# Kernel optimization log

Hardware: AMD Instinct MI355X
Metric: run time of the kernel (lower is better)

## Reference

```python
import jax, jax.numpy as jnp
import numpy as np

B, S, D, DH = 2, 2048, 1024, 64
H = D // DH
EPS = 1e-6

def rms_norm(x):
    # flax RMSNorm, use_scale=False: x / sqrt(mean(x^2) + eps)
    return x * jax.lax.rsqrt(jnp.mean(jnp.square(x), axis=-1, keepdims=True) + EPS)

def setup_inputs() -> dict:
    key = jax.random.key(0)
    ks = jax.random.split(key, 6)
    std = (1.0 / D) ** 0.5
    x = jax.random.normal(ks[0], (B, S, D), dtype=jnp.float32)
    Wq = jax.random.normal(ks[1], (D, D), dtype=jnp.float32) * std
    Wk = jax.random.normal(ks[2], (D, D), dtype=jnp.float32) * std
    Wv = jax.random.normal(ks[3], (D, D), dtype=jnp.float32) * std
    # output_proj is zero-initialized in the original; use small random so
    # backward through it is non-trivial for kernel correctness testing.
    Wo = jax.random.normal(ks[4], (D, D), dtype=jnp.float32) * std
    mask = jnp.tril(jnp.ones((S, S), dtype=bool))[None, None]  # causal [1,1,S,S]
    return {"x": x, "Wq": Wq, "Wk": Wk, "Wv": Wv, "Wo": Wo, "mask": mask}

def reference(x, Wq, Wk, Wv, Wo, mask):
    scale = (1.0 / DH) ** 0.5
    q = (x @ Wq).reshape(B, S, H, DH).transpose(0, 2, 1, 3)  # [B,H,S,DH]
    k = (x @ Wk).reshape(B, S, H, DH).transpose(0, 2, 1, 3)
    v = (x @ Wv).reshape(B, S, H, DH).transpose(0, 2, 1, 3)
    q = rms_norm(q)
    k = rms_norm(k)
    scores = jnp.einsum('bhsd,bhtd->bhst', q, k) * scale
    scores = jnp.where(mask, scores, jnp.finfo(scores.dtype).min)
    probs = jax.nn.softmax(scores, axis=-1)
    out = jnp.einsum('bhst,bhtd->bhsd', probs, v)
    out = out.transpose(0, 2, 1, 3).reshape(B, S, D)
    return out @ Wo
```

## Files before the change

kernel.cpp:

```cpp
#include <hip/hip_runtime.h>
#include <stdint.h>


typedef __attribute__((ext_vector_type(8))) short s16x8;
typedef __attribute__((ext_vector_type(4))) float fx4;
typedef __attribute__((ext_vector_type(4))) unsigned int ux4;
typedef __attribute__((ext_vector_type(2))) unsigned int ux2;

__device__ __forceinline__ unsigned short f2bf(float x) {
  unsigned u = __builtin_bit_cast(unsigned, x);
  u += 0x7fffu + ((u >> 16) & 1u);
  return (unsigned short)(u >> 16);
}
__device__ __forceinline__ float bf2f(unsigned short h) {
  return __builtin_bit_cast(float, (unsigned)h << 16);
}

__device__ __forceinline__ void gload_lds16(const void* g, void* l) {
  __builtin_amdgcn_global_load_lds(
      (const __attribute__((address_space(1))) unsigned int*)g,
      (__attribute__((address_space(3))) unsigned int*)l, 16, 0, 0);
}

__global__ void k_conv_bf16(const float* __restrict__ X,
                            unsigned short* __restrict__ Y, int n4) {
  int stride = gridDim.x * blockDim.x;
  for (int i = blockIdx.x * blockDim.x + threadIdx.x; i < n4; i += stride) {
    fx4 v = *(const fx4*)(X + (size_t)i * 4);
    ux2 o;
    o[0] = (unsigned)f2bf(v[0]) | ((unsigned)f2bf(v[1]) << 16);
    o[1] = (unsigned)f2bf(v[2]) | ((unsigned)f2bf(v[3]) << 16);
    *(ux2*)(Y + (size_t)i * 4) = o;
  }
}

__global__ void k_transpose_w(const float* __restrict__ W0, const float* __restrict__ W1,
                              const float* __restrict__ W2, const float* __restrict__ W3,
                              unsigned short* __restrict__ T0, unsigned short* __restrict__ T1,
                              unsigned short* __restrict__ T2, unsigned short* __restrict__ T3) {
  const float* W = blockIdx.z == 0 ? W0 : blockIdx.z == 1 ? W1 : blockIdx.z == 2 ? W2 : W3;
  unsigned short* T = blockIdx.z == 0 ? T0 : blockIdx.z == 1 ? T1 : blockIdx.z == 2 ? T2 : T3;
  __shared__ float t[32][33];
  int bx = blockIdx.x * 32, by = blockIdx.y * 32;
  int tx = threadIdx.x, ty = threadIdx.y;
#pragma unroll
  for (int i = 0; i < 32; i += 8)
    t[ty + i][tx] = W[(size_t)(by + ty + i) * 1024 + bx + tx];
  __syncthreads();
#pragma unroll
  for (int i = 0; i < 32; i += 8)
    T[(size_t)(bx + ty + i) * 1024 + by + tx] = f2bf(t[tx][ty + i]);
}

template <int OUTF32>
__global__ __launch_bounds__(256, 2)
void k_gemm_bt(const unsigned short* __restrict__ A,
               const unsigned short* __restrict__ W0,
               const unsigned short* __restrict__ W1,
               const unsigned short* __restrict__ W2,
               void* __restrict__ Cptr, int ldc) {
  __shared__ unsigned short As[128 * 64];
  __shared__ unsigned short Bs[128 * 64];
  const int tid = threadIdx.x;
  const int w = tid >> 6, l = tid & 63;
  const int lr = l & 15, lg = l >> 4;
  const int wm = w >> 1, wn = w & 1;
  const int m0 = blockIdx.x * 128;
  const int nt = blockIdx.y;
  const unsigned short* Bt = (nt < 8) ? W0 : (nt < 16) ? W1 : W2;
  const int n0 = (nt & 7) * 128;

  fx4 acc[4][4] = {};

  const int srow = w * 8 + (l >> 3);
  const int skb  = ((l & 7) ^ (l >> 3)) * 8;
  const unsigned short* aB = A  + (size_t)(m0 + srow) * 1024 + skb;
  const unsigned short* bB = Bt + (size_t)(n0 + srow) * 1024 + skb;
  unsigned short* aD = &As[w * 512];
  unsigned short* bD = &Bs[w * 512];
  const int rdswz = (l & 7) << 4;

  for (int kt = 0; kt < 1024; kt += 64) {
    __syncthreads();
#pragma unroll
    for (int j = 0; j < 4; ++j) {
      gload_lds16(aB + j * 32768 + kt, aD + j * 2048);
      gload_lds16(bB + j * 32768 + kt, bD + j * 2048);
    }
    __syncthreads();
#pragma unroll
    for (int ks = 0; ks < 2; ++ks) {
      const int kb = (ks * 64 + lg * 16) ^ rdswz;
      s16x8 af[4], bf[4];
#pragma unroll
      for (int mf = 0; mf < 4; ++mf)
        af[mf] = *(const s16x8*)((const char*)As + (wm * 64 + mf * 16 + lr) * 128 + kb);
#pragma unroll
      for (int nf = 0; nf < 4; ++nf)
        bf[nf] = *(const s16x8*)((const char*)Bs + (wn * 64 + nf * 16 + lr) * 128 + kb);
#pragma unroll
      for (int mf = 0; mf < 4; ++mf)
#pragma unroll
        for (int nf = 0; nf < 4; ++nf)
          acc[mf][nf] = __builtin_amdgcn_mfma_f32_16x16x32_bf16(af[mf], bf[nf], acc[mf][nf], 0, 0, 0);
    }
  }

  const int gn = nt * 128 + wn * 64;
  const int gm = m0 + wm * 64;
#pragma unroll
  for (int mf = 0; mf < 4; ++mf)
#pragma unroll
    for (int r = 0; r < 4; ++r) {
      int row = gm + mf * 16 + lg * 4 + r;
      if (OUTF32) {
        float* C = (float*)Cptr + (size_t)row * ldc + gn;
#pragma unroll
        for (int nf = 0; nf < 4; ++nf) C[nf * 16 + lr] = acc[mf][nf][r];
      } else {
        unsigned short* C = (unsigned short*)Cptr + (size_t)row * ldc + gn;
#pragma unroll
        for (int nf = 0; nf < 4; ++nf) C[nf * 16 + lr] = f2bf(acc[mf][nf][r]);
      }
    }
}

__global__ __launch_bounds__(256)
void k_rms_split(const unsigned short* __restrict__ QKV,
                 unsigned short* __restrict__ qn, unsigned short* __restrict__ kn,
                 unsigned short* __restrict__ vb) {
  int t = blockIdx.x * 256 + threadIdx.x;
  int unit = t >> 3, sl = t & 7;
  int tz = unit >> 16;
  int r = unit & 0xffff;
  int bs = r >> 4, h = r & 15;
  const unsigned short* src = QKV + (size_t)bs * 3072 + tz * 1024 + h * 64 + sl * 8;
  ux4 dv = *(const ux4*)src;
  float f[8];
#pragma unroll
  for (int i = 0; i < 4; ++i) {
    f[2 * i]     = bf2f((unsigned short)(dv[i] & 0xffff));
    f[2 * i + 1] = bf2f((unsigned short)(dv[i] >> 16));
  }
  float ss = 0.f;
#pragma unroll
  for (int i = 0; i < 8; ++i) ss += f[i] * f[i];
  ss += __shfl_xor(ss, 1);
  ss += __shfl_xor(ss, 2);
  ss += __shfl_xor(ss, 4);
  float scale = 1.0f;
  if (tz != 2) {
    scale = rsqrtf(ss * (1.0f / 64.0f) + 1e-6f);
    if (tz == 0) scale *= 0.18033688f;
  }
  ux4 o;
#pragma unroll
  for (int i = 0; i < 4; ++i)
    o[i] = (unsigned)f2bf(f[2 * i] * scale) | ((unsigned)f2bf(f[2 * i + 1] * scale) << 16);
  int b = bs >> 11, s = bs & 2047;
  unsigned short* dst = (tz == 0 ? qn : tz == 1 ? kn : vb)
                        + ((size_t)((b << 4) + h) * 2048 + s) * 64 + sl * 8;
  *(ux4*)dst = o;
}

__global__ __launch_bounds__(256, 2)
void k_attn(const unsigned short* __restrict__ Q,
            const unsigned short* __restrict__ K,
            const unsigned short* __restrict__ V,
            unsigned short* __restrict__ O) {
  __shared__ unsigned short Ks[2][64 * 64];
  __shared__ unsigned short Vt[2][64 * 72];
  __shared__ unsigned short Ps[4][16 * 72];

  const int id = blockIdx.x;
  const int bh = id & 31;
  const int pairIdx = id >> 5;
  const int tid = threadIdx.x;
  const int w = tid >> 6, l = tid & 63;
  const int lr = l & 15, lg = l >> 4;
  const int b = bh >> 4, h = bh & 15;

  const unsigned short* Kb = K + (size_t)bh * 2048 * 64;
  const unsigned short* Vb = V + (size_t)bh * 2048 * 64;

  const int ksrow = w * 8 + (l >> 3);
  const int kskb = ((l & 7) ^ (l >> 3)) * 8;
  const int vkvp = tid & 31;
  const int vdhg = tid >> 5;
  const int rdswz = (l & 7) << 4;
  const float FMAX = 11.5415603f;

#pragma unroll 1
  for (int pi = 0; pi < 2; ++pi) {
    const int tq = pi ? (31 - pairIdx) : pairIdx;
    const int q0 = tq * 64;
    const int qw = q0 + w * 16;
    const int nt = tq + 1;

    const unsigned short* Qb = Q + ((size_t)bh * 2048 + qw) * 64;
    s16x8 aq[2];
    aq[0] = *(const s16x8*)(Qb + lr * 64 + lg * 8);
    aq[1] = *(const s16x8*)(Qb + lr * 64 + 32 + lg * 8);

    fx4 oacc[4] = {};
    float lsum[4] = {0.f, 0.f, 0.f, 0.f};

    ux4 va0, va1;
#pragma unroll
    for (int j = 0; j < 2; ++j)
      gload_lds16(Kb + (size_t)(j * 32 + ksrow) * 64 + kskb, &Ks[0][j * 2048 + w * 512]);
    va0 = *(const ux4*)(Vb + (size_t)(2 * vkvp) * 64 + vdhg * 8);
    va1 = *(const ux4*)(Vb + (size_t)(2 * vkvp + 1) * 64 + vdhg * 8);
    {
      union { ux4 v; unsigned short u[8]; } a0, a1;
      a0.v = va0; a1.v = va1;
#pragma unroll
      for (int i = 0; i < 8; ++i)
        *(unsigned*)((char*)&Vt[0][0] + (vdhg * 8 + i) * 144 + vkvp * 4) =
            (unsigned)a0.u[i] | ((unsigned)a1.u[i] << 16);
    }
    __syncthreads();

#pragma unroll 1
    for (int t = 0; t < nt; ++t) {
      const int cur = t & 1;
      const int kv0 = t * 64;
      const bool pre = (t + 1 < nt);
      if (pre) {
        const int kvn = kv0 + 64;
#pragma unroll
        for (int j = 0; j < 2; ++j)
          gload_lds16(Kb + (size_t)(kvn + j * 32 + ksrow) * 64 + kskb,
                      &Ks[cur ^ 1][j * 2048 + w * 512]);
        va0 = *(const ux4*)(Vb + (size_t)(kvn + 2 * vkvp) * 64 + vdhg * 8);
        va1 = *(const ux4*)(Vb + (size_t)(kvn + 2 * vkvp + 1) * 64 + vdhg * 8);
      }
      fx4 sc[4] = {};
#pragma unroll
      for (int ks = 0; ks < 2; ++ks) {
        const int kb = (ks * 64 + lg * 16) ^ rdswz;
#pragma unroll
        for (int nf = 0; nf < 4; ++nf) {
          s16x8 bk = *(const s16x8*)((const char*)&Ks[cur][0] + (nf * 16 + lr) * 128 + kb);
          sc[nf] = __builtin_amdgcn_mfma_f32_16x16x32_bf16(aq[ks], bk, sc[nf], 0, 0, 0);
        }
      }
      if (t == nt - 1) {
#pragma unroll
        for (int nf = 0; nf < 4; ++nf)
#pragma unroll
          for (int r = 0; r < 4; ++r) {
            int gq = qw + lg * 4 + r;
            int gk = kv0 + nf * 16 + lr;
            if (gk > gq) sc[nf][r] = -3.0e38f;
          }
      }
      unsigned short* pw = &Ps[w][0];
#pragma unroll
      for (int r = 0; r < 4; ++r) {
        float p0 = __builtin_amdgcn_exp2f(sc[0][r] - FMAX);
        float p1 = __builtin_amdgcn_exp2f(sc[1][r] - FMAX);
        float p2 = __builtin_amdgcn_exp2f(sc[2][r] - FMAX);
        float p3 = __builtin_amdgcn_exp2f(sc[3][r] - FMAX);
        lsum[r] += (p0 + p1) + (p2 + p3);
        unsigned short* prow = pw + (lg * 4 + r) * 72;
        prow[lr]      = f2bf(p0);
        prow[lr + 16] = f2bf(p1);
        prow[lr + 32] = f2bf(p2);
        prow[lr + 48] = f2bf(p3);
      }
#pragma unroll
      for (int ks = 0; ks < 2; ++ks) {
        s16x8 pa = *(const s16x8*)((const char*)pw + lr * 144 + ks * 64 + lg * 16);
#pragma unroll
        for (int nf = 0; nf < 4; ++nf) {
          s16x8 bv = *(const s16x8*)((const char*)&Vt[cur][0] + (nf * 16 + lr) * 144 + ks * 64 + lg * 16);
          oacc[nf] = __builtin_amdgcn_mfma_f32_16x16x32_bf16(pa, bv, oacc[nf], 0, 0, 0);
        }
      }
      if (pre) {
        union { ux4 v; unsigned short u[8]; } a0, a1;
        a0.v = va0; a1.v = va1;
#pragma unroll
        for (int i = 0; i < 8; ++i)
          *(unsigned*)((char*)&Vt[cur ^ 1][0] + (vdhg * 8 + i) * 144 + vkvp * 4) =
              (unsigned)a0.u[i] | ((unsigned)a1.u[i] << 16);
      }
      __syncthreads();
    }

#pragma unroll
    for (int r = 0; r < 4; ++r) {
      float s = lsum[r];
      s += __shfl_xor(s, 1);
      s += __shfl_xor(s, 2);
      s += __shfl_xor(s, 4);
      s += __shfl_xor(s, 8);
      float inv = 1.0f / s;
      int gq = qw + lg * 4 + r;
      unsigned short* orow = O + ((size_t)(b * 2048 + gq)) * 1024 + h * 64;
#pragma unroll
      for (int nf = 0; nf < 4; ++nf)
        orow[nf * 16 + lr] = f2bf(oacc[nf][r] * inv);
    }
  }
}

extern "C" void kernel_launch(void* const* d_in, const int* in_sizes, int n_in,
                              void* d_out, int out_size, void* d_ws, size_t ws_size,
                              hipStream_t stream) {
  const float* x  = (const float*)d_in[0];
  const float* Wq = (const float*)d_in[1];
  const float* Wk = (const float*)d_in[2];
  const float* Wv = (const float*)d_in[3];
  const float* Wo = (const float*)d_in[4];

  char* ws = (char*)d_ws;
  unsigned short* xb   = (unsigned short*)(ws);
  unsigned short* WqT  = (unsigned short*)(ws + (8ll  << 20));
  unsigned short* WkT  = (unsigned short*)(ws + (10ll << 20));
  unsigned short* WvT  = (unsigned short*)(ws + (12ll << 20));
  unsigned short* WoT  = (unsigned short*)(ws + (14ll << 20));
  unsigned short* QKV  = (unsigned short*)(ws + (16ll << 20));
  unsigned short* qn   = (unsigned short*)(ws + (40ll << 20));
  unsigned short* kn   = (unsigned short*)(ws + (48ll << 20));
  unsigned short* vb   = (unsigned short*)(ws + (56ll << 20));
  unsigned short* attn = (unsigned short*)(ws + (64ll << 20));

  k_conv_bf16<<<1024, 256, 0, stream>>>(x, xb, 4096 * 1024 / 4);
  k_transpose_w<<<dim3(32, 32, 4), dim3(32, 8), 0, stream>>>(Wq, Wk, Wv, Wo, WqT, WkT, WvT, WoT);
  k_gemm_bt<0><<<dim3(32, 24), 256, 0, stream>>>(xb, WqT, WkT, WvT, (void*)QKV, 3072);
  k_rms_split<<<6144, 256, 0, stream>>>(QKV, qn, kn, vb);
  k_attn<<<512, 256, 0, stream>>>(qn, kn, vb, attn);
  k_gemm_bt<1><<<dim3(32, 8), 256, 0, stream>>>(attn, WoT, WoT, WoT, d_out, 1024);
}
```

Baseline: 114.5 us.

## Fuse RMS norm into QKV GEMM epilogue and retile attention to 128-row query blocks

The QKV GEMM epilogue now computes the per-head RMS norm in registers and writes normalized Q/K and V directly in head-major layout, so the separate k_rms_split pass and the QKV intermediate buffer are gone. The attention kernel now handles one 128-row query tile per block, each wave owning 32 rows, in place of paired 64-row tiles. Tiles are ordered to balance the causal work. P and V^T in LDS use XOR swizzling in place of padding. This cuts a kernel launch and a round trip through global memory and increases K/V reuse per load. In exchange it raises register pressure in attention and lowers the number of blocks per unit of work.

```diff
diff --git a/kernel.cpp b/kernel.cpp
--- a/kernel.cpp
+++ b/kernel.cpp
@@ -52,13 +52,15 @@
     T[(size_t)(bx + ty + i) * 1024 + by + tx] = f2bf(t[tx][ty + i]);
 }
 
-template <int OUTF32>
+template <int MODE>
 __global__ __launch_bounds__(256, 2)
 void k_gemm_bt(const unsigned short* __restrict__ A,
                const unsigned short* __restrict__ W0,
                const unsigned short* __restrict__ W1,
                const unsigned short* __restrict__ W2,
-               void* __restrict__ Cptr, int ldc) {
+               void* __restrict__ Cptr, int ldc,
+               unsigned short* __restrict__ qn, unsigned short* __restrict__ kn,
+               unsigned short* __restrict__ vb) {
   __shared__ unsigned short As[128 * 64];
   __shared__ unsigned short Bs[128 * 64];
   const int tid = threadIdx.x;
@@ -106,61 +108,44 @@
     }
   }
 
-  const int gn = nt * 128 + wn * 64;
-  const int gm = m0 + wm * 64;
-#pragma unroll
-  for (int mf = 0; mf < 4; ++mf)
-#pragma unroll
-    for (int r = 0; r < 4; ++r) {
-      int row = gm + mf * 16 + lg * 4 + r;
-      if (OUTF32) {
+  if (MODE == 1) {
+    const int gn = nt * 128 + wn * 64;
+    const int gm = m0 + wm * 64;
+#pragma unroll
+    for (int mf = 0; mf < 4; ++mf)
+#pragma unroll
+      for (int r = 0; r < 4; ++r) {
+        int row = gm + mf * 16 + lg * 4 + r;
         float* C = (float*)Cptr + (size_t)row * ldc + gn;
 #pragma unroll
         for (int nf = 0; nf < 4; ++nf) C[nf * 16 + lr] = acc[mf][nf][r];
-      } else {
-        unsigned short* C = (unsigned short*)Cptr + (size_t)row * ldc + gn;
-#pragma unroll
-        for (int nf = 0; nf < 4; ++nf) C[nf * 16 + lr] = f2bf(acc[mf][nf][r]);
-      }
-    }
-}
-
-__global__ __launch_bounds__(256)
-void k_rms_split(const unsigned short* __restrict__ QKV,
-                 unsigned short* __restrict__ qn, unsigned short* __restrict__ kn,
-                 unsigned short* __restrict__ vb) {
-  int t = blockIdx.x * 256 + threadIdx.x;
-  int unit = t >> 3, sl = t & 7;
-  int tz = unit >> 16;
-  int r = unit & 0xffff;
-  int bs = r >> 4, h = r & 15;
-  const unsigned short* src = QKV + (size_t)bs * 3072 + tz * 1024 + h * 64 + sl * 8;
-  ux4 dv = *(const ux4*)src;
-  float f[8];
-#pragma unroll
-  for (int i = 0; i < 4; ++i) {
-    f[2 * i]     = bf2f((unsigned short)(dv[i] & 0xffff));
-    f[2 * i + 1] = bf2f((unsigned short)(dv[i] >> 16));
-  }
-  float ss = 0.f;
-#pragma unroll
-  for (int i = 0; i < 8; ++i) ss += f[i] * f[i];
-  ss += __shfl_xor(ss, 1);
-  ss += __shfl_xor(ss, 2);
-  ss += __shfl_xor(ss, 4);
-  float scale = 1.0f;
-  if (tz != 2) {
-    scale = rsqrtf(ss * (1.0f / 64.0f) + 1e-6f);
-    if (tz == 0) scale *= 0.18033688f;
-  }
-  ux4 o;
-#pragma unroll
-  for (int i = 0; i < 4; ++i)
-    o[i] = (unsigned)f2bf(f[2 * i] * scale) | ((unsigned)f2bf(f[2 * i + 1] * scale) << 16);
-  int b = bs >> 11, s = bs & 2047;
-  unsigned short* dst = (tz == 0 ? qn : tz == 1 ? kn : vb)
-                        + ((size_t)((b << 4) + h) * 2048 + s) * 64 + sl * 8;
-  *(ux4*)dst = o;
+      }
+  } else {
+    const int tz = nt >> 3;
+    const int h  = ((nt & 7) << 1) | wn;
+    const int gm = m0 + wm * 64;
+    unsigned short* base = tz == 0 ? qn : tz == 1 ? kn : vb;
+    const float cmul = (tz == 0) ? 0.18033688f : 1.0f;
+#pragma unroll
+    for (int mf = 0; mf < 4; ++mf)
+#pragma unroll
+      for (int r = 0; r < 4; ++r) {
+        int m = gm + mf * 16 + lg * 4 + r;
+        float ss = 0.f;
+#pragma unroll
+        for (int nf = 0; nf < 4; ++nf) ss += acc[mf][nf][r] * acc[mf][nf][r];
+        ss += __shfl_xor(ss, 1);
+        ss += __shfl_xor(ss, 2);
+        ss += __shfl_xor(ss, 4);
+        ss += __shfl_xor(ss, 8);
+        float scale = (tz == 2) ? 1.0f : rsqrtf(ss * (1.0f / 64.0f) + 1e-6f) * cmul;
+        int b = m >> 11, s = m & 2047;
+        unsigned short* dst = base + ((size_t)(((b << 4) + h) * 2048 + s)) * 64;
+#pragma unroll
+        for (int nf = 0; nf < 4; ++nf)
+          dst[nf * 16 + lr] = f2bf(acc[mf][nf][r] * scale);
+      }
+  }
 }
 
 __global__ __launch_bounds__(256, 2)
@@ -169,141 +154,168 @@
             const unsigned short* __restrict__ V,
             unsigned short* __restrict__ O) {
   __shared__ unsigned short Ks[2][64 * 64];
-  __shared__ unsigned short Vt[2][64 * 72];
-  __shared__ unsigned short Ps[4][16 * 72];
+  __shared__ unsigned short Vt[2][64 * 64];
+  __shared__ unsigned short Ps[4][32 * 64];
 
   const int id = blockIdx.x;
   const int bh = id & 31;
-  const int pairIdx = id >> 5;
+  const int traw = id >> 5;
+  const int tq = (traw < 8) ? traw : 23 - traw;
+  const int q0 = tq * 128;
   const int tid = threadIdx.x;
   const int w = tid >> 6, l = tid & 63;
   const int lr = l & 15, lg = l >> 4;
   const int b = bh >> 4, h = bh & 15;
+  const int qw = q0 + w * 32;
 
   const unsigned short* Kb = K + (size_t)bh * 2048 * 64;
   const unsigned short* Vb = V + (size_t)bh * 2048 * 64;
+  const unsigned short* Qb = Q + ((size_t)bh * 2048 + qw) * 64;
+
+  s16x8 aq[2][2];
+#pragma unroll
+  for (int mf = 0; mf < 2; ++mf)
+#pragma unroll
+    for (int ks = 0; ks < 2; ++ks)
+      aq[mf][ks] = *(const s16x8*)(Qb + (mf * 16 + lr) * 64 + ks * 32 + lg * 8);
+
+  fx4 oacc[2][4] = {};
+  float lsum[2][4] = {{0.f, 0.f, 0.f, 0.f}, {0.f, 0.f, 0.f, 0.f}};
 
   const int ksrow = w * 8 + (l >> 3);
   const int kskb = ((l & 7) ^ (l >> 3)) * 8;
-  const int vkvp = tid & 31;
-  const int vdhg = tid >> 5;
-  const int rdswz = (l & 7) << 4;
+  const int vhalf = (tid & 31) >> 4;
+  const int va_   = tid & 15;
+  const int vdhg  = tid >> 5;
+  const int vr0   = vhalf * 32 + va_;
+  const int rdswz = (lr & 7) << 4;
   const float FMAX = 11.5415603f;
 
+  const int ntl = 2 * (tq + 1);
+
+  ux4 va0, va1;
+#pragma unroll
+  for (int j = 0; j < 2; ++j)
+    gload_lds16(Kb + (size_t)(j * 32 + ksrow) * 64 + kskb, &Ks[0][j * 2048 + w * 512]);
+  va0 = *(const ux4*)(Vb + (size_t)vr0 * 64 + vdhg * 8);
+  va1 = *(const ux4*)(Vb + (size_t)(vr0 + 16) * 64 + vdhg * 8);
+  {
+    union { ux4 v; unsigned short u[8]; } a0, a1;
+    a0.v = va0; a1.v = va1;
+#pragma unroll
+    for (int i = 0; i < 8; ++i) {
+      int dh = vdhg * 8 + i;
+      *(unsigned*)((char*)&Vt[0][0] + dh * 128 + ((vhalf * 64 + va_ * 4) ^ (i << 4))) =
+          (unsigned)a0.u[i] | ((unsigned)a1.u[i] << 16);
+    }
+  }
+  __syncthreads();
+
 #pragma unroll 1
-  for (int pi = 0; pi < 2; ++pi) {
-    const int tq = pi ? (31 - pairIdx) : pairIdx;
-    const int q0 = tq * 64;
-    const int qw = q0 + w * 16;
-    const int nt = tq + 1;
-
-    const unsigned short* Qb = Q + ((size_t)bh * 2048 + qw) * 64;
-    s16x8 aq[2];
-    aq[0] = *(const s16x8*)(Qb + lr * 64 + lg * 8);
-    aq[1] = *(const s16x8*)(Qb + lr * 64 + 32 + lg * 8);
-
-    fx4 oacc[4] = {};
-    float lsum[4] = {0.f, 0.f, 0.f, 0.f};
-
-    ux4 va0, va1;
-#pragma unroll
-    for (int j = 0; j < 2; ++j)
-      gload_lds16(Kb + (size_t)(j * 32 + ksrow) * 64 + kskb, &Ks[0][j * 2048 + w * 512]);
-    va0 = *(const ux4*)(Vb + (size_t)(2 * vkvp) * 64 + vdhg * 8);
-    va1 = *(const ux4*)(Vb + (size_t)(2 * vkvp + 1) * 64 + vdhg * 8);
-    {
+  for (int t = 0; t < ntl; ++t) {
+    const int cur = t & 1;
+    const int kv0 = t * 64;
+    const bool pre = (t + 1 < ntl);
+    if (pre) {
+      const int kvn = kv0 + 64;
+#pragma unroll
+      for (int j = 0; j < 2; ++j)
+        gload_lds16(Kb + (size_t)(kvn + j * 32 + ksrow) * 64 + kskb,
+                    &Ks[cur ^ 1][j * 2048 + w * 512]);
+      va0 = *(const ux4*)(Vb + (size_t)(kvn + vr0) * 64 + vdhg * 8);
+      va1 = *(const ux4*)(Vb + (size_t)(kvn + vr0 + 16) * 64 + vdhg * 8);
+    }
+    if (kv0 <= qw + 31) {
+      fx4 sc[2][4] = {};
+#pragma unroll
+      for (int ks = 0; ks < 2; ++ks) {
+        const int kb = (ks * 64 + lg * 16) ^ rdswz;
+#pragma unroll
+        for (int nf = 0; nf < 4; ++nf) {
+          s16x8 bk = *(const s16x8*)((const char*)&Ks[cur][0] + (nf * 16 + lr) * 128 + kb);
+#pragma unroll
+          for (int mf = 0; mf < 2; ++mf)
+            sc[mf][nf] = __builtin_amdgcn_mfma_f32_16x16x32_bf16(aq[mf][ks], bk, sc[mf][nf], 0, 0, 0);
+        }
+      }
+      if (kv0 + 63 > qw) {
+#pragma unroll
+        for (int mf = 0; mf < 2; ++mf)
+#pragma unroll
+          for (int nf = 0; nf < 4; ++nf)
+#pragma unroll
+            for (int r = 0; r < 4; ++r) {
+              int gq = qw + mf * 16 + lg * 4 + r;
+              int gk = kv0 + nf * 16 + lr;
+              if (gk > gq) sc[mf][nf][r] = -3.0e38f;
+            }
+      }
+      char* pw = (char*)&Ps[w][0];
+#pragma unroll
+      for (int mf = 0; mf < 2; ++mf)
+#pragma unroll
+        for (int r = 0; r < 4; ++r) {
+          float p0 = __builtin_amdgcn_exp2f(sc[mf][0][r] - FMAX);
+          float p1 = __builtin_amdgcn_exp2f(sc[mf][1][r] - FMAX);
+          float p2 = __builtin_amdgcn_exp2f(sc[mf][2][r] - FMAX);
+          float p3 = __builtin_amdgcn_exp2f(sc[mf][3][r] - FMAX);
+          lsum[mf][r] += (p0 + p1) + (p2 + p3);
+          int row = mf * 16 + lg * 4 + r;
+          char* pb = pw + row * 128;
+          int swz = (row & 7) << 4;
+          *(unsigned*)(pb + ((4 * lr) ^ swz))      = (unsigned)f2bf(p0) | ((unsigned)f2bf(p1) << 16);
+          *(unsigned*)(pb + ((64 + 4 * lr) ^ swz)) = (unsigned)f2bf(p2) | ((unsigned)f2bf(p3) << 16);
+        }
+#pragma unroll
+      for (int ks = 0; ks < 2; ++ks) {
+        s16x8 pa[2], bv[4];
+#pragma unroll
+        for (int mf = 0; mf < 2; ++mf) {
+          int row = mf * 16 + lr;
+          pa[mf] = *(const s16x8*)(pw + row * 128 + ((ks * 64 + lg * 16) ^ ((row & 7) << 4)));
+        }
+#pragma unroll
+        for (int nf = 0; nf < 4; ++nf) {
+          int row = nf * 16 + lr;
+          bv[nf] = *(const s16x8*)((const char*)&Vt[cur][0] + row * 128 +
+                                   ((ks * 64 + lg * 16) ^ ((row & 7) << 4)));
+        }
+#pragma unroll
+        for (int mf = 0; mf < 2; ++mf)
+#pragma unroll
+          for (int nf = 0; nf < 4; ++nf)
+            oacc[mf][nf] = __builtin_amdgcn_mfma_f32_16x16x32_bf16(pa[mf], bv[nf], oacc[mf][nf], 0, 0, 0);
+      }
+    }
+    if (pre) {
       union { ux4 v; unsigned short u[8]; } a0, a1;
       a0.v = va0; a1.v = va1;
 #pragma unroll
-      for (int i = 0; i < 8; ++i)
-        *(unsigned*)((char*)&Vt[0][0] + (vdhg * 8 + i) * 144 + vkvp * 4) =
+      for (int i = 0; i < 8; ++i) {
+        int dh = vdhg * 8 + i;
+        *(unsigned*)((char*)&Vt[cur ^ 1][0] + dh * 128 + ((vhalf * 64 + va_ * 4) ^ (i << 4))) =
             (unsigned)a0.u[i] | ((unsigned)a1.u[i] << 16);
+      }
     }
     __syncthreads();
-
-#pragma unroll 1
-    for (int t = 0; t < nt; ++t) {
-      const int cur = t & 1;
-      const int kv0 = t * 64;
-      const bool pre = (t + 1 < nt);
-      if (pre) {
-        const int kvn = kv0 + 64;
-#pragma unroll
-        for (int j = 0; j < 2; ++j)
-          gload_lds16(Kb + (size_t)(kvn + j * 32 + ksrow) * 64 + kskb,
-                      &Ks[cur ^ 1][j * 2048 + w * 512]);
-        va0 = *(const ux4*)(Vb + (size_t)(kvn + 2 * vkvp) * 64 + vdhg * 8);
-        va1 = *(const ux4*)(Vb + (size_t)(kvn + 2 * vkvp + 1) * 64 + vdhg * 8);
-      }
-      fx4 sc[4] = {};
-#pragma unroll
-      for (int ks = 0; ks < 2; ++ks) {
-        const int kb = (ks * 64 + lg * 16) ^ rdswz;
-#pragma unroll
-        for (int nf = 0; nf < 4; ++nf) {
-          s16x8 bk = *(const s16x8*)((const char*)&Ks[cur][0] + (nf * 16 + lr) * 128 + kb);
-          sc[nf] = __builtin_amdgcn_mfma_f32_16x16x32_bf16(aq[ks], bk, sc[nf], 0, 0, 0);
-        }
-      }
-      if (t == nt - 1) {
-#pragma unroll
-        for (int nf = 0; nf < 4; ++nf)
-#pragma unroll
-          for (int r = 0; r < 4; ++r) {
-            int gq = qw + lg * 4 + r;
-            int gk = kv0 + nf * 16 + lr;
-            if (gk > gq) sc[nf][r] = -3.0e38f;
-          }
-      }
-      unsigned short* pw = &Ps[w][0];
-#pragma unroll
-      for (int r = 0; r < 4; ++r) {
-        float p0 = __builtin_amdgcn_exp2f(sc[0][r] - FMAX);
-        float p1 = __builtin_amdgcn_exp2f(sc[1][r] - FMAX);
-        float p2 = __builtin_amdgcn_exp2f(sc[2][r] - FMAX);
-        float p3 = __builtin_amdgcn_exp2f(sc[3][r] - FMAX);
-        lsum[r] += (p0 + p1) + (p2 + p3);
-        unsigned short* prow = pw + (lg * 4 + r) * 72;
-        prow[lr]      = f2bf(p0);
-        prow[lr + 16] = f2bf(p1);
-        prow[lr + 32] = f2bf(p2);
-        prow[lr + 48] = f2bf(p3);
-      }
-#pragma unroll
-      for (int ks = 0; ks < 2; ++ks) {
-        s16x8 pa = *(const s16x8*)((const char*)pw + lr * 144 + ks * 64 + lg * 16);
-#pragma unroll
-        for (int nf = 0; nf < 4; ++nf) {
-          s16x8 bv = *(const s16x8*)((const char*)&Vt[cur][0] + (nf * 16 + lr) * 144 + ks * 64 + lg * 16);
-          oacc[nf] = __builtin_amdgcn_mfma_f32_16x16x32_bf16(pa, bv, oacc[nf], 0, 0, 0);
-        }
-      }
-      if (pre) {
-        union { ux4 v; unsigned short u[8]; } a0, a1;
-        a0.v = va0; a1.v = va1;
-#pragma unroll
-        for (int i = 0; i < 8; ++i)
-          *(unsigned*)((char*)&Vt[cur ^ 1][0] + (vdhg * 8 + i) * 144 + vkvp * 4) =
-              (unsigned)a0.u[i] | ((unsigned)a1.u[i] << 16);
-      }
-      __syncthreads();
-    }
-
+  }
+
+#pragma unroll
+  for (int mf = 0; mf < 2; ++mf)
 #pragma unroll
     for (int r = 0; r < 4; ++r) {
-      float s = lsum[r];
+      float s = lsum[mf][r];
       s += __shfl_xor(s, 1);
       s += __shfl_xor(s, 2);
       s += __shfl_xor(s, 4);
       s += __shfl_xor(s, 8);
       float inv = 1.0f / s;
-      int gq = qw + lg * 4 + r;
+      int gq = qw + mf * 16 + lg * 4 + r;
       unsigned short* orow = O + ((size_t)(b * 2048 + gq)) * 1024 + h * 64;
 #pragma unroll
       for (int nf = 0; nf < 4; ++nf)
-        orow[nf * 16 + lr] = f2bf(oacc[nf][r] * inv);
-    }
-  }
+        orow[nf * 16 + lr] = f2bf(oacc[mf][nf][r] * inv);
+    }
 }
 
 extern "C" void kernel_launch(void* const* d_in, const int* in_sizes, int n_in,
@@ -321,16 +333,14 @@
   unsigned short* WkT  = (unsigned short*)(ws + (10ll << 20));
   unsigned short* WvT  = (unsigned short*)(ws + (12ll << 20));
   unsigned short* WoT  = (unsigned short*)(ws + (14ll << 20));
-  unsigned short* QKV  = (unsigned short*)(ws + (16ll << 20));
-  unsigned short* qn   = (unsigned short*)(ws + (40ll << 20));
-  unsigned short* kn   = (unsigned short*)(ws + (48ll << 20));
-  unsigned short* vb   = (unsigned short*)(ws + (56ll << 20));
-  unsigned short* attn = (unsigned short*)(ws + (64ll << 20));
+  unsigned short* qn   = (unsigned short*)(ws + (16ll << 20));
+  unsigned short* kn   = (unsigned short*)(ws + (24ll << 20));
+  unsigned short* vb   = (unsigned short*)(ws + (32ll << 20));
+  unsigned short* attn = (unsigned short*)(ws + (40ll << 20));
 
   k_conv_bf16<<<1024, 256, 0, stream>>>(x, xb, 4096 * 1024 / 4);
   k_transpose_w<<<dim3(32, 32, 4), dim3(32, 8), 0, stream>>>(Wq, Wk, Wv, Wo, WqT, WkT, WvT, WoT);
-  k_gemm_bt<0><<<dim3(32, 24), 256, 0, stream>>>(xb, WqT, WkT, WvT, (void*)QKV, 3072);
-  k_rms_split<<<6144, 256, 0, stream>>>(QKV, qn, kn, vb);
+  k_gemm_bt<2><<<dim3(32, 24), 256, 0, stream>>>(xb, WqT, WkT, WvT, nullptr, 0, qn, kn, vb);
   k_attn<<<512, 256, 0, stream>>>(qn, kn, vb, attn);
-  k_gemm_bt<1><<<dim3(32, 8), 256, 0, stream>>>(attn, WoT, WoT, WoT, d_out, 1024);
-}
+  k_gemm_bt<1><<<dim3(32, 8), 256, 0, stream>>>(attn, WoT, WoT, WoT, d_out, 1024, nullptr, nullptr, nullptr);
+}
```

Result: no change. 115.6 us (+1.0%).
